# Optimization experiments

Hardware: AMD Instinct MI355X
Metric: run time of the kernel (lower is better)

Reference implementation:

```python
import jax, jax.numpy as jnp
import numpy as np
import math

B, N, D, RANK = 16, 65536, 8, 2
IN_SIZE, OUT_SIZE = 4096, 4096
TWO_PI = 2.0 * math.pi


def setup_inputs() -> dict:
    key = jax.random.key(0)
    k = jax.random.split(key, 6)
    x = jax.random.normal(k[0], (B, IN_SIZE), jnp.float32)
    # means live in index space: dim0 in [0, OUT_SIZE), dim1 in [0, IN_SIZE)
    means = jax.random.uniform(k[1], (B, N, RANK), jnp.float32) * jnp.array(
        [OUT_SIZE - 1, IN_SIZE - 1], jnp.float32)
    sigmas = jax.random.uniform(k[2], (B, N), jnp.float32) * 2.0 + 0.5  # positive stddevs
    values = jax.random.normal(k[3], (B, N), jnp.float32)
    bias = jax.random.normal(k[4], (OUT_SIZE,), jnp.float32) * 0.1
    noise = jax.random.normal(k[5], (B, N, D, RANK), jnp.float32)  # reparam noise (torch.randn in sample())
    return {"x": x, "means": means, "sigmas": sigmas, "values": values,
            "bias": bias, "noise": noise}


def reference(x, means, sigmas, values, bias, noise):
    # --- sample(): d reparameterized MVN samples per (mean, sigma) -> [B,N,D,RANK]
    samples = noise * sigmas[:, :, None, None] + means[:, :, None, :]
    # --- densities(): isotropic Gaussian pdf of samples under their own MVN -> [B,N,D]
    diff = samples - means[:, :, None, :]
    products = jnp.sum(diff * diff, axis=-1)              # squared distances [B,N,D]
    s2 = (sigmas * sigmas)[:, :, None]                    # sigma^2, [B,N,1]
    den = jnp.sqrt((TWO_PI ** RANK) * s2 ** RANK)
    probs = jnp.exp(-products / (2.0 * s2)) / den         # [B,N,D]
    # normalize proportions over the D samples of each tuple
    probs = probs / jnp.sum(probs, axis=2, keepdims=True)
    # --- round and clamp to integer indices in w_shape = (OUT_SIZE, IN_SIZE)
    upper = jnp.array([OUT_SIZE - 1, IN_SIZE - 1], jnp.float32)
    ints = jnp.clip(jnp.round(samples), 0.0, upper).astype(jnp.int32)  # [B,N,D,2]
    # --- weighted values, flattened to N*D sparse entries per batch element
    vals = (values[:, :, None] * probs).reshape(B, N * D)
    out_idx = ints[..., 0].reshape(B, N * D)
    in_idx = ints[..., 1].reshape(B, N * D)
    # --- segmented sparse matvec: y[b, o] += vals * x[b, i]
    # (equivalent to the sorted grouped dot-product loop in the torch code)
    def one(xb, oi, ii, vb):
        return jnp.zeros((OUT_SIZE,), x.dtype).at[oi].add(vb * xb[ii])
    y = jax.vmap(one)(x, out_idx, in_idx, vals)           # [B, OUT_SIZE]
    return y + bias
```

## Files before the change

### kernel.cpp

```cpp
#include <hip/hip_runtime.h>
#include <math.h>

#define BB 16
#define NN 65536
#define DD 8
#define OUT_SIZE 4096
#define IN_SIZE 4096

#define BLOCKS_PER_B 32
#define NC (NN / BLOCKS_PER_B)
#define BLOCK_THREADS 1024

__global__ void init_out(const float* __restrict__ bias, float* __restrict__ y) {
    int i = blockIdx.x * blockDim.x + threadIdx.x;
    y[i] = bias[i & (OUT_SIZE - 1)];
}

__global__ __launch_bounds__(BLOCK_THREADS, 4)
void hyper_scatter(const float* __restrict__ x,
                   const float* __restrict__ means,
                   const float* __restrict__ sigmas,
                   const float* __restrict__ values,
                   const float* __restrict__ noise,
                   float* __restrict__ y) {
    __shared__ float ys[OUT_SIZE];
    __shared__ float xs[IN_SIZE];

    const int b     = blockIdx.x / BLOCKS_PER_B;
    const int chunk = blockIdx.x % BLOCKS_PER_B;
    const int tid   = threadIdx.x;
    const float* xb = x + (size_t)b * IN_SIZE;

    ((float4*)ys)[tid] = make_float4(0.f, 0.f, 0.f, 0.f);
    ((float4*)xs)[tid] = ((const float4*)xb)[tid];
    __syncthreads();

    const int n0 = chunk * NC;

    float2 mean[2]; float sigma[2], value[2];
    float4 nzv[2][4];
    #pragma unroll
    for (int t = 0; t < 2; ++t) {
        const size_t base = (size_t)b * NN + (size_t)(n0 + tid + t * BLOCK_THREADS);
        mean[t]  = ((const float2*)means)[base];
        sigma[t] = sigmas[base];
        value[t] = values[base];
        const float4* np4 = (const float4*)(noise + base * (size_t)(DD * 2));
        nzv[t][0] = np4[0]; nzv[t][1] = np4[1];
        nzv[t][2] = np4[2]; nzv[t][3] = np4[3];
    }

    float p[2][DD];
    int   oi[2][DD], ii[2][DD];
    float wscale[2];
    #pragma unroll
    for (int t = 0; t < 2; ++t) {
        const float nr[DD * 2] = {
            nzv[t][0].x, nzv[t][0].y, nzv[t][0].z, nzv[t][0].w,
            nzv[t][1].x, nzv[t][1].y, nzv[t][1].z, nzv[t][1].w,
            nzv[t][2].x, nzv[t][2].y, nzv[t][2].z, nzv[t][2].w,
            nzv[t][3].x, nzv[t][3].y, nzv[t][3].z, nzv[t][3].w };
        const float neg_inv_2s2 = -0.5f / (sigma[t] * sigma[t]);
        float psum = 0.f;
        #pragma unroll
        for (int d = 0; d < DD; ++d) {
            float s0 = __fadd_rn(__fmul_rn(nr[2 * d],     sigma[t]), mean[t].x);
            float s1 = __fadd_rn(__fmul_rn(nr[2 * d + 1], sigma[t]), mean[t].y);
            float d0 = s0 - mean[t].x;
            float d1 = s1 - mean[t].y;
            float q  = d0 * d0 + d1 * d1;
            float pd = __expf(q * neg_inv_2s2);
            p[t][d] = pd;
            psum += pd;
            oi[t][d] = (int)fminf(fmaxf(rintf(s0), 0.f), (float)(OUT_SIZE - 1));
            ii[t][d] = (int)fminf(fmaxf(rintf(s1), 0.f), (float)(IN_SIZE - 1));
        }
        wscale[t] = value[t] / psum;
    }

    float xv[2][DD];
    #pragma unroll
    for (int t = 0; t < 2; ++t)
        #pragma unroll
        for (int d = 0; d < DD; ++d)
            xv[t][d] = (d & 1) ? xb[ii[t][d]] : xs[ii[t][d]];

    #pragma unroll
    for (int t = 0; t < 2; ++t) {
        float v[DD];
        #pragma unroll
        for (int d = 0; d < DD; ++d) v[d] = p[t][d] * xv[t][d];

        bool deadO[DD];
        deadO[0] = false;
        #pragma unroll
        for (int d = 1; d < DD; ++d) {
            bool found = false;
            #pragma unroll
            for (int j = 0; j < d; ++j) {
                bool m = (!deadO[j]) && (oi[t][j] == oi[t][d]);
                if (m) v[j] += v[d];
                found = found || m;
            }
            deadO[d] = found;
        }
        #pragma unroll
        for (int d = 0; d < DD; ++d) {
            if (!deadO[d]) atomicAdd(&ys[oi[t][d]], wscale[t] * v[d]);
        }
    }
    __syncthreads();

    float* yb = y + (size_t)b * OUT_SIZE;
    #pragma unroll
    for (int o = tid; o < OUT_SIZE; o += BLOCK_THREADS) {
        unsafeAtomicAdd(&yb[o], ys[o]);
    }
}

extern "C" void kernel_launch(void* const* d_in, const int* in_sizes, int n_in,
                              void* d_out, int out_size, void* d_ws, size_t ws_size,
                              hipStream_t stream) {
    const float* x      = (const float*)d_in[0];
    const float* means  = (const float*)d_in[1];
    const float* sigmas = (const float*)d_in[2];
    const float* values = (const float*)d_in[3];
    const float* bias   = (const float*)d_in[4];
    const float* noise  = (const float*)d_in[5];
    float* y = (float*)d_out;

    init_out<<<(BB * OUT_SIZE) / 256, 256, 0, stream>>>(bias, y);
    hyper_scatter<<<BB * BLOCKS_PER_B, BLOCK_THREADS, 0, stream>>>(
        x, means, sigmas, values, noise, y);
}
```

Measured before the change: 127.8 us.

## Halve block size and software-pipeline per-tuple loads across iterations

Block size drops from 1024 to 512 threads, so each thread now walks 4 tuples in a loop. The next tuple's means, sigma, value and noise are prefetched into registers while the current one is computed, overlapping global load latency with exp, index math and LDS atomics. This trades thread-level parallelism for instruction-level overlap and adds register pressure from the prefetch buffers. A leftover empty scope block is dead code.

```diff
diff --git a/kernel.cpp b/kernel.cpp
--- a/kernel.cpp
+++ b/kernel.cpp
@@ -9,7 +9,8 @@
 
 #define BLOCKS_PER_B 32
 #define NC (NN / BLOCKS_PER_B)
-#define BLOCK_THREADS 1024
+#define BLOCK_THREADS 512
+#define ITERS (NC / BLOCK_THREADS)
 
 __global__ void init_out(const float* __restrict__ bias, float* __restrict__ y) {
     int i = blockIdx.x * blockDim.x + threadIdx.x;
@@ -31,65 +32,72 @@
     const int tid   = threadIdx.x;
     const float* xb = x + (size_t)b * IN_SIZE;
 
-    ((float4*)ys)[tid] = make_float4(0.f, 0.f, 0.f, 0.f);
-    ((float4*)xs)[tid] = ((const float4*)xb)[tid];
+    ((float4*)ys)[tid]                 = make_float4(0.f, 0.f, 0.f, 0.f);
+    ((float4*)ys)[tid + BLOCK_THREADS] = make_float4(0.f, 0.f, 0.f, 0.f);
+    ((float4*)xs)[tid]                 = ((const float4*)xb)[tid];
+    ((float4*)xs)[tid + BLOCK_THREADS] = ((const float4*)xb)[tid + BLOCK_THREADS];
     __syncthreads();
 
-    const int n0 = chunk * NC;
+    const size_t base0 = (size_t)b * NN + (size_t)(chunk * NC + tid);
 
-    float2 mean[2]; float sigma[2], value[2];
-    float4 nzv[2][4];
+    float2 mean  = ((const float2*)means)[base0];
+    float  sigma = sigmas[base0];
+    float  value = values[base0];
+    {
+        const float4* np4 = (const float4*)(noise + base0 * (size_t)(DD * 2));
+    }
+    const float4* np4_0 = (const float4*)(noise + base0 * (size_t)(DD * 2));
+    float4 nz0 = np4_0[0], nz1 = np4_0[1], nz2 = np4_0[2], nz3 = np4_0[3];
+
     #pragma unroll
-    for (int t = 0; t < 2; ++t) {
-        const size_t base = (size_t)b * NN + (size_t)(n0 + tid + t * BLOCK_THREADS);
-        mean[t]  = ((const float2*)means)[base];
-        sigma[t] = sigmas[base];
-        value[t] = values[base];
-        const float4* np4 = (const float4*)(noise + base * (size_t)(DD * 2));
-        nzv[t][0] = np4[0]; nzv[t][1] = np4[1];
-        nzv[t][2] = np4[2]; nzv[t][3] = np4[3];
-    }
+    for (int it = 0; it < ITERS; ++it) {
+        const float2 m  = mean;
+        const float  sg = sigma;
+        const float  val = value;
+        const float4 c0 = nz0, c1 = nz1, c2 = nz2, c3 = nz3;
 
-    float p[2][DD];
-    int   oi[2][DD], ii[2][DD];
-    float wscale[2];
-    #pragma unroll
-    for (int t = 0; t < 2; ++t) {
+        if (it + 1 < ITERS) {
+            const size_t nb = base0 + (size_t)((it + 1) * BLOCK_THREADS);
+            mean  = ((const float2*)means)[nb];
+            sigma = sigmas[nb];
+            value = values[nb];
+            const float4* q4 = (const float4*)(noise + nb * (size_t)(DD * 2));
+            nz0 = q4[0]; nz1 = q4[1]; nz2 = q4[2]; nz3 = q4[3];
+        }
+
         const float nr[DD * 2] = {
-            nzv[t][0].x, nzv[t][0].y, nzv[t][0].z, nzv[t][0].w,
-            nzv[t][1].x, nzv[t][1].y, nzv[t][1].z, nzv[t][1].w,
-            nzv[t][2].x, nzv[t][2].y, nzv[t][2].z, nzv[t][2].w,
-            nzv[t][3].x, nzv[t][3].y, nzv[t][3].z, nzv[t][3].w };
-        const float neg_inv_2s2 = -0.5f / (sigma[t] * sigma[t]);
+            c0.x, c0.y, c0.z, c0.w,
+            c1.x, c1.y, c1.z, c1.w,
+            c2.x, c2.y, c2.z, c2.w,
+            c3.x, c3.y, c3.z, c3.w };
+
+        const float neg_inv_2s2 = -0.5f / (sg * sg);
+        float p[DD];
+        int   oi[DD], ii[DD];
         float psum = 0.f;
         #pragma unroll
         for (int d = 0; d < DD; ++d) {
-            float s0 = __fadd_rn(__fmul_rn(nr[2 * d],     sigma[t]), mean[t].x);
-            float s1 = __fadd_rn(__fmul_rn(nr[2 * d + 1], sigma[t]), mean[t].y);
-            float d0 = s0 - mean[t].x;
-            float d1 = s1 - mean[t].y;
+            float s0 = __fadd_rn(__fmul_rn(nr[2 * d],     sg), m.x);
+            float s1 = __fadd_rn(__fmul_rn(nr[2 * d + 1], sg), m.y);
+            float d0 = s0 - m.x;
+            float d1 = s1 - m.y;
             float q  = d0 * d0 + d1 * d1;
             float pd = __expf(q * neg_inv_2s2);
-            p[t][d] = pd;
+            p[d] = pd;
             psum += pd;
-            oi[t][d] = (int)fminf(fmaxf(rintf(s0), 0.f), (float)(OUT_SIZE - 1));
-            ii[t][d] = (int)fminf(fmaxf(rintf(s1), 0.f), (float)(IN_SIZE - 1));
+            oi[d] = (int)fminf(fmaxf(rintf(s0), 0.f), (float)(OUT_SIZE - 1));
+            ii[d] = (int)fminf(fmaxf(rintf(s1), 0.f), (float)(IN_SIZE - 1));
         }
-        wscale[t] = value[t] / psum;
-    }
+        const float wscale = val / psum;
 
-    float xv[2][DD];
-    #pragma unroll
-    for (int t = 0; t < 2; ++t)
+        float xv[DD];
         #pragma unroll
         for (int d = 0; d < DD; ++d)
-            xv[t][d] = (d & 1) ? xb[ii[t][d]] : xs[ii[t][d]];
+            xv[d] = (d & 1) ? xb[ii[d]] : xs[ii[d]];
 
-    #pragma unroll
-    for (int t = 0; t < 2; ++t) {
         float v[DD];
         #pragma unroll
-        for (int d = 0; d < DD; ++d) v[d] = p[t][d] * xv[t][d];
+        for (int d = 0; d < DD; ++d) v[d] = p[d] * xv[d];
 
         bool deadO[DD];
         deadO[0] = false;
@@ -98,15 +106,15 @@
             bool found = false;
             #pragma unroll
             for (int j = 0; j < d; ++j) {
-                bool m = (!deadO[j]) && (oi[t][j] == oi[t][d]);
-                if (m) v[j] += v[d];
-                found = found || m;
+                bool mch = (!deadO[j]) && (oi[j] == oi[d]);
+                if (mch) v[j] += v[d];
+                found = found || mch;
             }
             deadO[d] = found;
         }
         #pragma unroll
         for (int d = 0; d < DD; ++d) {
-            if (!deadO[d]) atomicAdd(&ys[oi[t][d]], wscale[t] * v[d]);
+            if (!deadO[d]) atomicAdd(&ys[oi[d]], wscale * v[d]);
         }
     }
     __syncthreads();
```

New measurement: 130.3 us. About the same (+2.0%).
